# Kernel tuning notes

Measured on AMD Instinct MI355X. Metric: run time of the kernel, lower is better.

## Reference

```python
import jax, jax.numpy as jnp
import numpy as np

B, S, IN_DIM = 8, 2048, 8
EMB, HEADS, NCLS = 512, 8, 3
HDIM = EMB // HEADS
HALF = EMB // 2


def setup_inputs() -> dict:
    key = jax.random.key(0)
    ks = jax.random.split(key, 16)
    g = lambda k, shp, fan_in: jax.random.normal(k, shp, jnp.float32) / np.sqrt(fan_in)
    return {
        "features": jax.random.normal(ks[0], (B, S, IN_DIM), jnp.float32),
        "timestamps": jax.random.uniform(ks[1], (B, S, 1), jnp.float32),
        # FeatureEmbedding
        "Wf": g(ks[2], (IN_DIM, EMB), IN_DIM), "bf": jnp.zeros((EMB,), jnp.float32),
        # Time2Vec
        "Wl": g(ks[3], (1, HALF), 1), "bl": jnp.zeros((HALF,), jnp.float32),
        "Wp": g(ks[4], (1, HALF), 1), "bp": jnp.zeros((HALF,), jnp.float32),
        # TimeAwareAttention
        "Wq": g(ks[5], (EMB, EMB), EMB), "bq": jnp.zeros((EMB,), jnp.float32),
        "Wk": g(ks[6], (EMB, EMB), EMB), "bk": jnp.zeros((EMB,), jnp.float32),
        "Wv": g(ks[7], (EMB, EMB), EMB), "bv": jnp.zeros((EMB,), jnp.float32),
        "Wo": g(ks[8], (EMB, EMB), EMB), "bo": jnp.zeros((EMB,), jnp.float32),
        "time_decay": jnp.ones((1,), jnp.float32),
        # Classifier MLP (dropout is identity in eval)
        "W1": g(ks[9], (EMB, EMB // 2), EMB), "b1": jnp.zeros((EMB // 2,), jnp.float32),
        "W2": g(ks[10], (EMB // 2, NCLS), EMB // 2), "b2": jnp.zeros((NCLS,), jnp.float32),
    }


def reference(features, timestamps, Wf, bf, Wl, bl, Wp, bp,
              Wq, bq, Wk, bk, Wv, bv, Wo, bo, time_decay, W1, b1, W2, b2):
    # embeddings: feature linear + Time2Vec(linear || sin(linear))
    feat_emb = features @ Wf + bf                              # [B,S,E]
    time_emb = jnp.concatenate(
        [timestamps @ Wl + bl, jnp.sin(timestamps @ Wp + bp)], axis=-1)
    x = feat_emb + time_emb                                    # [B,S,E]

    # pairwise time-decay weights: exp(-decay * |t_i - t_j|)  [B,S,S]
    t = timestamps[..., 0]
    decay = jnp.exp(-time_decay[0] * jnp.abs(t[:, :, None] - t[:, None, :]))

    def split_heads(y):  # [B,S,E] -> [B,H,S,D]
        return y.reshape(B, S, HEADS, HDIM).transpose(0, 2, 1, 3)

    q = split_heads(x @ Wq + bq)
    k = split_heads(x @ Wk + bk)
    v = split_heads(x @ Wv + bv)

    scores = jnp.einsum('bhsd,bhtd->bhst', q, k) / np.sqrt(HDIM).astype(np.float32)
    scores = scores * decay[:, None, :, :]                     # elementwise decay bias
    attn = jax.nn.softmax(scores, axis=-1)
    out = jnp.einsum('bhst,bhtd->bhsd', attn, v)               # [B,H,S,D]
    out = out.transpose(0, 2, 1, 3).reshape(B, S, EMB)
    out = out @ Wo + bo

    h = out[:, -1, :]                                          # last token
    h = jax.nn.relu(h @ W1 + b1)
    logits = h @ W2 + b2                                       # [B,NCLS]
    return logits
```

## Files before the change

kernel.cpp:

```cpp
#include <hip/hip_runtime.h>
#include <hip/hip_bf16.h>
#include <math.h>

#define B 8
#define S 2048
#define IN_DIM 8
#define EMB 512
#define HEADS 8
#define HDIM 64
#define HALF 256
#define NCLS 3
#define NCHUNK 32
#define CT 64
#define SINSTRIDE 260

#define WS_KQ    0
#define WS_COEF1 32768
#define WS_PM    33536
#define WS_PS    66304
#define WS_POP   590592

__global__ __launch_bounds__(256) void k_head(
    const float* __restrict__ feat, const float* __restrict__ ts,
    const float* __restrict__ Wf, const float* __restrict__ bf,
    const float* __restrict__ Wl, const float* __restrict__ bl,
    const float* __restrict__ Wp, const float* __restrict__ bp,
    const float* __restrict__ Wq, const float* __restrict__ bq,
    const float* __restrict__ Wk, const float* __restrict__ bk,
    float* __restrict__ ws)
{
    const int h = blockIdx.x;
    const int b = blockIdx.y;
    const int bh = b*HEADS + h;
    const int tid = threadIdx.x;
    __shared__ float xl[EMB];
    __shared__ __align__(16) float qc[HDIM];
    __shared__ float kq[EMB];
    __shared__ float red[4][64];
    __shared__ float red10[4][12];

    {
        const float tl = ts[b*S + (S-1)];
        float fv[IN_DIM];
        #pragma unroll
        for (int i = 0; i < IN_DIM; ++i) fv[i] = feat[(b*S + (S-1))*IN_DIM + i];
        #pragma unroll
        for (int r = 0; r < 2; ++r) {
            const int e = tid + r*256;
            float acc = bf[e];
            #pragma unroll
            for (int i = 0; i < IN_DIM; ++i) acc += fv[i]*Wf[i*EMB + e];
            if (r == 0) acc += tl*Wl[e] + bl[e];
            else        acc += __sinf(tl*Wp[e-HALF] + bp[e-HALF]);
            xl[e] = acc;
        }
    }
    __syncthreads();
    {
        const int eo = tid & 63, jq = tid >> 6;
        float acc = (jq == 0) ? bq[h*HDIM + eo] : 0.f;
        #pragma unroll 8
        for (int j = jq*128; j < jq*128 + 128; ++j)
            acc += xl[j]*Wq[j*EMB + h*HDIM + eo];
        red[jq][eo] = acc;
    }
    __syncthreads();
    if (tid < HDIM) qc[tid] = red[0][tid]+red[1][tid]+red[2][tid]+red[3][tid];
    __syncthreads();
    {
        #pragma unroll
        for (int r = 0; r < 2; ++r) {
            const int j = tid + r*256;
            const float4* wr = (const float4*)(Wk + j*EMB + h*HDIM);
            const float4* qv = (const float4*)qc;
            float acc = 0.f;
            #pragma unroll
            for (int k = 0; k < 16; ++k) {
                const float4 w = wr[k], q4 = qv[k];
                acc += w.x*q4.x + w.y*q4.y + w.z*q4.z + w.w*q4.w;
            }
            kq[j] = acc;
            if (j >= HALF) ws[WS_KQ + bh*EMB + j] = acc;
        }
    }
    __syncthreads();
    {
        float a[IN_DIM] = {0.f,0.f,0.f,0.f,0.f,0.f,0.f,0.f};
        float c0 = 0.f, c1 = 0.f;
        #pragma unroll
        for (int r = 0; r < 2; ++r) {
            const int e = tid + r*256;
            const float kv = kq[e];
            #pragma unroll
            for (int i = 0; i < IN_DIM; ++i) a[i] += Wf[i*EMB + e]*kv;
            c0 += bf[e]*kv;
            if (r == 0) { c0 += bl[e]*kv; c1 += Wl[e]*kv; }
        }
        if (tid < HDIM) c0 += qc[tid]*bk[h*HDIM + tid];
        #pragma unroll
        for (int off = 32; off >= 1; off >>= 1) {
            #pragma unroll
            for (int i = 0; i < IN_DIM; ++i) a[i] += __shfl_xor(a[i], off, 64);
            c0 += __shfl_xor(c0, off, 64);
            c1 += __shfl_xor(c1, off, 64);
        }
        const int wid = tid >> 6, lane = tid & 63;
        if (lane == 0) {
            #pragma unroll
            for (int i = 0; i < IN_DIM; ++i) red10[wid][i] = a[i];
            red10[wid][8] = c0; red10[wid][9] = c1;
        }
        __syncthreads();
        if (tid < 10)
            ws[WS_COEF1 + bh*12 + tid] =
                red10[0][tid]+red10[1][tid]+red10[2][tid]+red10[3][tid];
    }
}

__global__ __launch_bounds__(256) void k_part(
    const float* __restrict__ feat, const float* __restrict__ ts,
    const float* __restrict__ Wp, const float* __restrict__ bp,
    const float* __restrict__ tdp, float* __restrict__ ws)
{
    const int c = blockIdx.x;
    const int b = blockIdx.y;
    const int tid = threadIdx.x;
    const int t0 = c*CT;

    __shared__ __align__(16) float sin_l[CT*SINSTRIDE];
    __shared__ __align__(16) float kqh[HEADS][256];
    __shared__ __align__(16) float w_l[CT*8];
    __shared__ float tv_l[CT];
    __shared__ float f_l[CT*9];
    __shared__ float cf[96];

    if (tid < CT) tv_l[tid] = ts[b*S + t0 + tid];
    for (int idx = tid; idx < CT*IN_DIM; idx += 256) {
        const int tt = idx >> 3, i = idx & 7;
        f_l[tt*9 + i] = feat[(b*S + t0 + tt)*IN_DIM + i];
    }
    for (int idx = tid; idx < HEADS*256; idx += 256)
        ((float*)kqh)[idx] = ws[WS_KQ + (b*HEADS + (idx >> 8))*EMB + HALF + (idx & 255)];
    if (tid < 96) cf[tid] = ws[WS_COEF1 + b*96 + tid];
    const float tl = ts[b*S + (S-1)];
    const float td = tdp[0];
    __syncthreads();

    {
        const float wj = Wp[tid], bj = bp[tid];
        #pragma unroll 4
        for (int tt = 0; tt < CT; ++tt)
            sin_l[tt*SINSTRIDE + tid] = __sinf(tv_l[tt]*wj + bj);
    }
    __syncthreads();

    const int t = tid & 63, h0 = tid >> 6;
    const float tv = tv_l[t];
    float fv[IN_DIM];
    #pragma unroll
    for (int i = 0; i < IN_DIM; ++i) fv[i] = f_l[t*9 + i];
    const float dec = __expf(-td*fabsf(tl - tv));
    float sc[2];
    {
        float acc0 = 0.f, acc1 = 0.f;
        const float4* srow = (const float4*)(sin_l + t*SINSTRIDE);
        const float4* kq0 = (const float4*)&kqh[h0][0];
        const float4* kq1 = (const float4*)&kqh[h0+4][0];
        #pragma unroll 4
        for (int j4 = 0; j4 < 64; ++j4) {
            const float4 sv = srow[j4];
            const float4 ka = kq0[j4], kb = kq1[j4];
            acc0 += sv.x*ka.x + sv.y*ka.y + sv.z*ka.z + sv.w*ka.w;
            acc1 += sv.x*kb.x + sv.y*kb.y + sv.z*kb.z + sv.w*kb.w;
        }
        #pragma unroll
        for (int p = 0; p < 2; ++p) {
            const int h = h0 + p*4;
            float base = cf[h*12+8] + tv*cf[h*12+9];
            #pragma unroll
            for (int i = 0; i < IN_DIM; ++i) base += fv[i]*cf[h*12+i];
            sc[p] = (base + ((p == 0) ? acc0 : acc1))*0.125f*dec;
        }
    }
    #pragma unroll
    for (int p = 0; p < 2; ++p) {
        const int h = h0 + p*4;
        float m = sc[p];
        #pragma unroll
        for (int off = 32; off >= 1; off >>= 1) m = fmaxf(m, __shfl_xor(m, off, 64));
        const float w = __expf(sc[p] - m);
        float Z = w, ta = w*tv;
        float fa[IN_DIM];
        #pragma unroll
        for (int i = 0; i < IN_DIM; ++i) fa[i] = w*fv[i];
        #pragma unroll
        for (int off = 32; off >= 1; off >>= 1) {
            Z  += __shfl_xor(Z,  off, 64);
            ta += __shfl_xor(ta, off, 64);
            #pragma unroll
            for (int i = 0; i < IN_DIM; ++i) fa[i] += __shfl_xor(fa[i], off, 64);
        }
        w_l[t*8 + h] = w;
        if (t == 0) {
            float* pm = ws + WS_PM + ((b*NCHUNK + c)*HEADS + h)*16;
            pm[0] = m; pm[1] = Z; pm[2] = ta;
            #pragma unroll
            for (int i = 0; i < IN_DIM; ++i) pm[3+i] = fa[i];
        }
    }
    __syncthreads();
    {
        const int j = tid;
        float accS[HEADS] = {0.f,0.f,0.f,0.f,0.f,0.f,0.f,0.f};
        const float4* wv4 = (const float4*)w_l;
        #pragma unroll 4
        for (int tt = 0; tt < CT; ++tt) {
            const float sv = sin_l[tt*SINSTRIDE + j];
            const float4 wa = wv4[tt*2], wb = wv4[tt*2+1];
            accS[0] += wa.x*sv; accS[1] += wa.y*sv; accS[2] += wa.z*sv; accS[3] += wa.w*sv;
            accS[4] += wb.x*sv; accS[5] += wb.y*sv; accS[6] += wb.z*sv; accS[7] += wb.w*sv;
        }
        const int base = WS_PS + ((b*NCHUNK + c)*HEADS)*256 + j;
        #pragma unroll
        for (int h = 0; h < HEADS; ++h) ws[base + h*256] = accS[h];
    }
}

__global__ __launch_bounds__(512) void k_ohw(
    const float* __restrict__ Wf, const float* __restrict__ bf,
    const float* __restrict__ Wl, const float* __restrict__ bl,
    const float* __restrict__ Wv, const float* __restrict__ bv,
    const float* __restrict__ Wo, float* __restrict__ ws)
{
    const int h = blockIdx.x;
    const int b = blockIdx.y;
    const int tid = threadIdx.x;
    __shared__ float pmL[NCHUNK][12];
    __shared__ float al[NCHUNK];
    __shared__ float cfL[10];
    __shared__ float wx[EMB];
    __shared__ float red[8][64];
    __shared__ __align__(16) float oh_c[HDIM];

    if (tid < NCHUNK*11)
        pmL[tid/11][tid%11] = ws[WS_PM + ((b*NCHUNK + tid/11)*HEADS + h)*16 + tid%11];
    __syncthreads();
    float m = pmL[0][0];
    #pragma unroll 8
    for (int c = 1; c < NCHUNK; ++c) m = fmaxf(m, pmL[c][0]);
    if (tid < NCHUNK) al[tid] = __expf(pmL[tid][0] - m);
    __syncthreads();
    float Z = 0.f;
    #pragma unroll 8
    for (int c = 0; c < NCHUNK; ++c) Z += al[c]*pmL[c][1];
    const float inv = 1.f/Z;
    if (tid < 9) {
        const int k = (tid == 8) ? 2 : 3 + tid;
        float acc = 0.f;
        #pragma unroll 8
        for (int c = 0; c < NCHUNK; ++c) acc += al[c]*pmL[c][k];
        cfL[(tid == 8) ? 8 : tid] = acc*inv;
    }
    __syncthreads();
    {
        const int e = tid;
        float val = bf[e];
        #pragma unroll
        for (int i = 0; i < IN_DIM; ++i) val += cfL[i]*Wf[i*EMB + e];
        if (e < HALF) {
            val += cfL[8]*Wl[e] + bl[e];
        } else {
            const int j = e - HALF;
            float acc = 0.f;
            #pragma unroll 8
            for (int c = 0; c < NCHUNK; ++c)
                acc += al[c]*ws[WS_PS + ((b*NCHUNK + c)*HEADS + h)*256 + j];
            val += acc*inv;
        }
        wx[e] = val;
    }
    __syncthreads();
    {
        const int eo = tid & 63, jq = tid >> 6;
        const int e = h*HDIM + eo;
        float acc = 0.f;
        #pragma unroll 8
        for (int j = jq*64; j < jq*64 + 64; ++j)
            acc += wx[j]*Wv[j*EMB + e];
        red[jq][eo] = acc;
    }
    __syncthreads();
    if (tid < 64) {
        float s = 0.f;
        #pragma unroll
        for (int q = 0; q < 8; ++q) s += red[q][tid];
        oh_c[tid] = s + bv[h*HDIM + tid];
    }
    __syncthreads();
    {
        const int e = tid;
        float acc = 0.f;
        #pragma unroll 8
        for (int d = 0; d < HDIM; ++d)
            acc += oh_c[d]*Wo[(h*HDIM + d)*EMB + e];
        ws[WS_POP + (b*HEADS + h)*EMB + e] = acc;
    }
}

__global__ __launch_bounds__(1024) void k_tail2(
    const float* __restrict__ bo,
    const float* __restrict__ W1, const float* __restrict__ b1,
    const float* __restrict__ W2, const float* __restrict__ b2,
    const float* __restrict__ ws, float* __restrict__ out)
{
    const int b = blockIdx.x;
    const int tid = threadIdx.x;
    __shared__ float opL[EMB];
    __shared__ float red[4][HALF];
    __shared__ float hhL[HALF];
    __shared__ float red3[4][3];

    if (tid < EMB) {
        float acc = bo[tid];
        #pragma unroll
        for (int h = 0; h < HEADS; ++h)
            acc += ws[WS_POP + (b*HEADS + h)*EMB + tid];
        opL[tid] = acc;
    }
    __syncthreads();
    {
        const int mm = tid & 255, jq = tid >> 8;
        float acc = 0.f;
        #pragma unroll 8
        for (int j = jq*128; j < jq*128 + 128; ++j)
            acc += opL[j]*W1[j*HALF + mm];
        red[jq][mm] = acc;
    }
    __syncthreads();
    if (tid < HALF)
        hhL[tid] = fmaxf(red[0][tid]+red[1][tid]+red[2][tid]+red[3][tid] + b1[tid], 0.f);
    __syncthreads();
    if (tid < HALF) {
        const float hv = hhL[tid];
        float p0 = hv*W2[tid*NCLS + 0];
        float p1 = hv*W2[tid*NCLS + 1];
        float p2 = hv*W2[tid*NCLS + 2];
        #pragma unroll
        for (int off = 32; off >= 1; off >>= 1) {
            p0 += __shfl_xor(p0, off, 64);
            p1 += __shfl_xor(p1, off, 64);
            p2 += __shfl_xor(p2, off, 64);
        }
        const int wid = tid >> 6;
        if ((tid & 63) == 0) { red3[wid][0] = p0; red3[wid][1] = p1; red3[wid][2] = p2; }
    }
    __syncthreads();
    if (tid < NCLS)
        out[b*NCLS + tid] = red3[0][tid]+red3[1][tid]+red3[2][tid]+red3[3][tid] + b2[tid];
}

extern "C" void kernel_launch(void* const* d_in, const int* in_sizes, int n_in,
                              void* d_out, int out_size, void* d_ws, size_t ws_size,
                              hipStream_t stream)
{
    const float* feat = (const float*)d_in[0];
    const float* ts   = (const float*)d_in[1];
    const float* Wf = (const float*)d_in[2];
    const float* bf = (const float*)d_in[3];
    const float* Wl = (const float*)d_in[4];
    const float* bl = (const float*)d_in[5];
    const float* Wp = (const float*)d_in[6];
    const float* bp = (const float*)d_in[7];
    const float* Wq = (const float*)d_in[8];
    const float* bq = (const float*)d_in[9];
    const float* Wk = (const float*)d_in[10];
    const float* bk = (const float*)d_in[11];
    const float* Wv = (const float*)d_in[12];
    const float* bv = (const float*)d_in[13];
    const float* Wo = (const float*)d_in[14];
    const float* bo = (const float*)d_in[15];
    const float* td = (const float*)d_in[16];
    const float* W1 = (const float*)d_in[17];
    const float* b1 = (const float*)d_in[18];
    const float* W2 = (const float*)d_in[19];
    const float* b2 = (const float*)d_in[20];
    float* ws = (float*)d_ws;
    float* out = (float*)d_out;

    hipLaunchKernelGGL(k_head,  dim3(HEADS, B),  dim3(256),  0, stream,
                       feat, ts, Wf, bf, Wl, bl, Wp, bp, Wq, bq, Wk, bk, ws);
    hipLaunchKernelGGL(k_part,  dim3(NCHUNK, B), dim3(256),  0, stream,
                       feat, ts, Wp, bp, td, ws);
    hipLaunchKernelGGL(k_ohw,   dim3(HEADS, B),  dim3(512),  0, stream,
                       Wf, bf, Wl, bl, Wv, bv, Wo, ws);
    hipLaunchKernelGGL(k_tail2, dim3(B),         dim3(1024), 0, stream,
                       bo, W1, b1, W2, b2, ws, out);
}
```

Baseline: 42.75 us.

## Push W1 projection into per-head kernel using linearity, shrink tail kernel

The per-head kernel now adds bo on head 0, multiplies its partial Wo output by W1, and writes a per-head partial of the hidden pre-activation. The tail kernel only sums the eight head partials, applies ReLU and does the tiny W2 projection. This uses the linearity of Wo and W1 to spread the W1 matvec across 64 blocks instead of 8, shortening the serial tail. In exchange W1 is read 8 times more in total and the k_ohw blocks do more work.

Result: no change. 43.57 us (+1.9%).

```diff
diff --git a/kernel.cpp b/kernel.cpp
--- a/kernel.cpp
+++ b/kernel.cpp
@@ -18,7 +18,7 @@
 #define WS_COEF1 32768
 #define WS_PM    33536
 #define WS_PS    66304
-#define WS_POP   590592
+#define WS_YH    590592
 
 __global__ __launch_bounds__(256) void k_head(
     const float* __restrict__ feat, const float* __restrict__ ts,
@@ -230,7 +230,9 @@
     const float* __restrict__ Wf, const float* __restrict__ bf,
     const float* __restrict__ Wl, const float* __restrict__ bl,
     const float* __restrict__ Wv, const float* __restrict__ bv,
-    const float* __restrict__ Wo, float* __restrict__ ws)
+    const float* __restrict__ Wo, const float* __restrict__ bo,
+    const float* __restrict__ W1, const float* __restrict__ b1,
+    float* __restrict__ ws)
 {
     const int h = blockIdx.x;
     const int b = blockIdx.y;
@@ -299,61 +301,56 @@
     __syncthreads();
     {
         const int e = tid;
-        float acc = 0.f;
+        float acc = (h == 0) ? bo[e] : 0.f;
         #pragma unroll 8
         for (int d = 0; d < HDIM; ++d)
             acc += oh_c[d]*Wo[(h*HDIM + d)*EMB + e];
-        ws[WS_POP + (b*HEADS + h)*EMB + e] = acc;
-    }
-}
-
-__global__ __launch_bounds__(1024) void k_tail2(
-    const float* __restrict__ bo,
-    const float* __restrict__ W1, const float* __restrict__ b1,
+        wx[e] = acc;
+    }
+    __syncthreads();
+    {
+        float* redW1 = (float*)red;
+        const int mm = tid & 255, jq = tid >> 8;
+        float acc = 0.f;
+        #pragma unroll 8
+        for (int j = jq*256; j < jq*256 + 256; ++j)
+            acc += wx[j]*W1[j*HALF + mm];
+        redW1[jq*HALF + mm] = acc;
+    }
+    __syncthreads();
+    if (tid < HALF) {
+        const float* redW1 = (const float*)red;
+        float y = redW1[tid] + redW1[HALF + tid];
+        if (h == 0) y += b1[tid];
+        ws[WS_YH + (b*HEADS + h)*HALF + tid] = y;
+    }
+}
+
+__global__ __launch_bounds__(256) void k_tail3(
     const float* __restrict__ W2, const float* __restrict__ b2,
     const float* __restrict__ ws, float* __restrict__ out)
 {
     const int b = blockIdx.x;
     const int tid = threadIdx.x;
-    __shared__ float opL[EMB];
-    __shared__ float red[4][HALF];
-    __shared__ float hhL[HALF];
     __shared__ float red3[4][3];
 
-    if (tid < EMB) {
-        float acc = bo[tid];
-        #pragma unroll
-        for (int h = 0; h < HEADS; ++h)
-            acc += ws[WS_POP + (b*HEADS + h)*EMB + tid];
-        opL[tid] = acc;
-    }
-    __syncthreads();
-    {
-        const int mm = tid & 255, jq = tid >> 8;
-        float acc = 0.f;
-        #pragma unroll 8
-        for (int j = jq*128; j < jq*128 + 128; ++j)
-            acc += opL[j]*W1[j*HALF + mm];
-        red[jq][mm] = acc;
-    }
-    __syncthreads();
-    if (tid < HALF)
-        hhL[tid] = fmaxf(red[0][tid]+red[1][tid]+red[2][tid]+red[3][tid] + b1[tid], 0.f);
-    __syncthreads();
-    if (tid < HALF) {
-        const float hv = hhL[tid];
-        float p0 = hv*W2[tid*NCLS + 0];
-        float p1 = hv*W2[tid*NCLS + 1];
-        float p2 = hv*W2[tid*NCLS + 2];
-        #pragma unroll
-        for (int off = 32; off >= 1; off >>= 1) {
-            p0 += __shfl_xor(p0, off, 64);
-            p1 += __shfl_xor(p1, off, 64);
-            p2 += __shfl_xor(p2, off, 64);
-        }
-        const int wid = tid >> 6;
-        if ((tid & 63) == 0) { red3[wid][0] = p0; red3[wid][1] = p1; red3[wid][2] = p2; }
-    }
+    float acc = 0.f;
+    #pragma unroll
+    for (int h = 0; h < HEADS; ++h)
+        acc += ws[WS_YH + (b*HEADS + h)*HALF + tid];
+    const float hv = fmaxf(acc, 0.f);
+
+    float p0 = hv*W2[tid*NCLS + 0];
+    float p1 = hv*W2[tid*NCLS + 1];
+    float p2 = hv*W2[tid*NCLS + 2];
+    #pragma unroll
+    for (int off = 32; off >= 1; off >>= 1) {
+        p0 += __shfl_xor(p0, off, 64);
+        p1 += __shfl_xor(p1, off, 64);
+        p2 += __shfl_xor(p2, off, 64);
+    }
+    const int wid = tid >> 6;
+    if ((tid & 63) == 0) { red3[wid][0] = p0; red3[wid][1] = p1; red3[wid][2] = p2; }
     __syncthreads();
     if (tid < NCLS)
         out[b*NCLS + tid] = red3[0][tid]+red3[1][tid]+red3[2][tid]+red3[3][tid] + b2[tid];
@@ -387,12 +384,12 @@
     float* ws = (float*)d_ws;
     float* out = (float*)d_out;
 
-    hipLaunchKernelGGL(k_head,  dim3(HEADS, B),  dim3(256),  0, stream,
+    hipLaunchKernelGGL(k_head,  dim3(HEADS, B),  dim3(256), 0, stream,
                        feat, ts, Wf, bf, Wl, bl, Wp, bp, Wq, bq, Wk, bk, ws);
-    hipLaunchKernelGGL(k_part,  dim3(NCHUNK, B), dim3(256),  0, stream,
+    hipLaunchKernelGGL(k_part,  dim3(NCHUNK, B), dim3(256), 0, stream,
                        feat, ts, Wp, bp, td, ws);
-    hipLaunchKernelGGL(k_ohw,   dim3(HEADS, B),  dim3(512),  0, stream,
-                       Wf, bf, Wl, bl, Wv, bv, Wo, ws);
-    hipLaunchKernelGGL(k_tail2, dim3(B),         dim3(1024), 0, stream,
-                       bo, W1, b1, W2, b2, ws, out);
-}
+    hipLaunchKernelGGL(k_ohw,   dim3(HEADS, B),  dim3(512), 0, stream,
+                       Wf, bf, Wl, bl, Wv, bv, Wo, bo, W1, b1, ws);
+    hipLaunchKernelGGL(k_tail3, dim3(B),         dim3(256), 0, stream,
+                       W2, b2, ws, out);
+}
```
